# Optimization experiments

Measured on AMD Instinct MI355X. Metric: run time of the kernel, lower is better.

## Reference

```python
import jax, jax.numpy as jnp
import numpy as np

N_ING, N_DIR = 100000, 50000
E = 1000000
H, D = 4, 16          # heads, per-head dim
HID = H * D           # 64
LAT, COND = 32, 8
F_ING, F_DIR = 16, 8
OUT_ING = 16


def _han_edge(x_src, x_dst, att_s, att_d, edge_index, n_dst):
    # HANConv per-edge-type attention message passing.
    src, dst = edge_index[0], edge_index[1]
    a = jax.nn.leaky_relu(
        jnp.einsum('nhd,hd->nh', x_src, att_s)[src]
        + jnp.einsum('nhd,hd->nh', x_dst, att_d)[dst],
        negative_slope=0.2)                               # [E, H]
    amax = jax.ops.segment_max(a, dst, num_segments=n_dst)
    ex = jnp.exp(a - amax[dst])
    denom = jax.ops.segment_sum(ex, dst, num_segments=n_dst)
    alpha = ex / (denom[dst] + 1e-16)                     # PyG softmax eps
    out = jax.ops.segment_sum(x_src[src] * alpha[:, :, None], dst,
                              num_segments=n_dst)         # [n_dst, H, D]
    return jax.nn.relu(out.reshape(n_dst, HID))


def _group(outs, q, Wk, bk):
    # HANConv semantic-level attention across edge types.
    s = jnp.stack(outs)                                   # [T, N, HID]
    score = jnp.tanh(s @ Wk + bk).mean(axis=1) @ q        # [T]
    attn = jax.nn.softmax(score)
    return jnp.einsum('t,tnf->nf', attn, s)


def setup_inputs() -> dict:
    key = jax.random.key(0)
    ks = jax.random.split(key, 32)
    def ei(k, n_src, n_dst):
        k1, k2 = jax.random.split(k)
        return jnp.stack([jax.random.randint(k1, (E,), 0, n_src),
                          jax.random.randint(k2, (E,), 0, n_dst)]).astype(jnp.int64)
    s = 0.1
    inp = {
        'x_ing': jax.random.normal(ks[0], (N_ING, F_ING), jnp.float32),
        'x_dir': jax.random.normal(ks[1], (N_DIR, F_DIR), jnp.float32),
        'cond':  jax.random.normal(ks[2], (COND,), jnp.float32),
        'eps':   jax.random.normal(ks[3], (1, LAT), jnp.float32),
        'ei_cooc':     ei(ks[4], N_ING, N_DIR),
        'ei_used':     ei(ks[5], N_ING, N_DIR),
        'ei_contains': ei(ks[6], N_DIR, N_ING),
        'ei_pairs':    ei(ks[7], N_DIR, N_DIR),
        'ei_follows':  ei(ks[8], N_DIR, N_DIR),
        # node-type projections
        'W_pi': jax.random.normal(ks[9],  (F_ING, HID)) * s,
        'b_pi': jnp.zeros((HID,)),
        'W_pd': jax.random.normal(ks[10], (F_DIR, HID)) * s,
        'b_pd': jnp.zeros((HID,)),
        # semantic attention
        'Wk': jax.random.normal(ks[21], (HID, HID)) * s,
        'bk': jnp.zeros((HID,)),
        'q':  jax.random.normal(ks[22], (HID,)) * s,
        # VAE heads (input: 2*HID + COND)
        'W_mu': jax.random.normal(ks[23], (2 * HID + COND, LAT)) * s,
        'b_mu': jnp.zeros((LAT,)),
        'W_lv': jax.random.normal(ks[24], (2 * HID + COND, LAT)) * s,
        'b_lv': jnp.zeros((LAT,)),
        # decoder (fc1 is dead code in the original forward)
        'W_fc3': jax.random.normal(ks[25], (LAT, HID)) * s,
        'b_fc3': jnp.zeros((HID,)),
        'W_fc2': jax.random.normal(ks[26], (HID, OUT_ING)) * s,
        'b_fc2': jnp.zeros((OUT_ING,)),
    }
    for i, name in enumerate(['cooc', 'used', 'contains', 'pairs', 'follows']):
        inp[f'as_{name}'] = jax.random.normal(ks[11 + i], (H, D)) * s
        inp[f'ad_{name}'] = jax.random.normal(ks[16 + i], (H, D)) * s
    return inp


def reference(x_ing, x_dir, cond, eps,
              ei_cooc, ei_used, ei_contains, ei_pairs, ei_follows,
              W_pi, b_pi, W_pd, b_pd,
              as_cooc, ad_cooc, as_used, ad_used, as_contains, ad_contains,
              as_pairs, ad_pairs, as_follows, ad_follows,
              Wk, bk, q, W_mu, b_mu, W_lv, b_lv,
              W_fc3, b_fc3, W_fc2, b_fc2):
    # node-type projections -> [N, H, D]
    h_ing = (x_ing @ W_pi + b_pi).reshape(N_ING, H, D)
    h_dir = (x_dir @ W_pd + b_pd).reshape(N_DIR, H, D)

    o_cooc = _han_edge(h_ing, h_dir, as_cooc, ad_cooc, ei_cooc, N_DIR)
    o_used = _han_edge(h_ing, h_dir, as_used, ad_used, ei_used, N_DIR)
    o_cont = _han_edge(h_dir, h_ing, as_contains, ad_contains, ei_contains, N_ING)
    o_pair = _han_edge(h_dir, h_dir, as_pairs, ad_pairs, ei_pairs, N_DIR)
    o_foll = _han_edge(h_dir, h_dir, as_follows, ad_follows, ei_follows, N_DIR)

    out_ing = _group([o_cont], q, Wk, bk)                       # [N_ING, HID]
    out_dir = _group([o_cooc, o_used, o_pair, o_foll], q, Wk, bk)

    ingre_pool = out_ing.mean(axis=0, keepdims=True)            # [1, HID]
    direc_pool = out_dir.mean(axis=0, keepdims=True)
    graph_repr = jnp.concatenate([ingre_pool, direc_pool, cond[None]], axis=1)

    mu = graph_repr @ W_mu + b_mu
    logvar = graph_repr @ W_lv + b_lv
    z = mu + eps * jnp.exp(0.5 * logvar)

    # decoder: fc1 branch is overwritten in the original; effective path below
    recon = jnp.tanh(jax.nn.relu(z @ W_fc3 + b_fc3) @ W_fc2 + b_fc2)  # [1, OUT_ING]
    return recon, mu, logvar
```

## Files before the change

kernel.cpp:

```cpp
#include <hip/hip_runtime.h>
#include <hip/hip_fp16.h>
#include <math.h>

#define N_ING 100000
#define N_DIR 50000
#define NE    1000000
#define NDST_TOTAL 300000
#define NBUCK 1172
#define BA    64
#define NBK   (5 * BA)
#define I4PT  (NE / 4)
#define PB_ING 384
#define PB_DIR 192
#define LOG2E 1.442695041f

typedef float v2f __attribute__((ext_vector_type(2)));
typedef __attribute__((ext_vector_type(8))) short bf16x8;
typedef __attribute__((ext_vector_type(4))) float f32x4;

__global__ __launch_bounds__(256) void kA_kernel(
    const int* __restrict__ e0, const int* __restrict__ e1,
    const int* __restrict__ e2, const int* __restrict__ e3,
    const int* __restrict__ e4, int* __restrict__ blockcnt,
    const float* __restrict__ x_ing, const float* __restrict__ W_pi,
    const float* __restrict__ b_pi,
    const float* __restrict__ as_cooc, const float* __restrict__ as_used,
    const float* __restrict__ ad_contains,
    unsigned* __restrict__ h8_ing, __half* __restrict__ s_ing,
    const float* __restrict__ x_dir, const float* __restrict__ W_pd,
    const float* __restrict__ b_pd,
    const float* __restrict__ ad_cooc, const float* __restrict__ ad_used,
    const float* __restrict__ as_contains, const float* __restrict__ as_pairs,
    const float* __restrict__ ad_pairs, const float* __restrict__ as_follows,
    const float* __restrict__ ad_follows,
    unsigned* __restrict__ h8_dir, __half* __restrict__ s_dir)
{
    __shared__ int hist[NBUCK];
    __shared__ float sW[16 * 64];
    __shared__ float sbb[64];
    __shared__ float satt[7 * 64];
    __shared__ float sx[4][16];
    __shared__ float srow[4][64];

    const int bid = blockIdx.x;
    const int tid = threadIdx.x;
    if (bid < NBK) {
        const int type = bid / BA, blk = bid % BA;
        const int* ei = type == 0 ? e0 : type == 1 ? e1 : type == 2 ? e2
                      : type == 3 ? e3 : e4;
        const int base = type == 0 ? 0 : type == 1 ? 50000 : type == 2 ? 100000
                       : type == 3 ? 200000 : 250000;
        for (int i = tid; i < NBUCK; i += 256) hist[i] = 0;
        __syncthreads();
        const int4* d4 = (const int4*)(ei + NE);
        for (int i = blk * 256 + tid; i < I4PT; i += BA * 256) {
            int4 d = d4[i];
            atomicAdd(&hist[(base + d.x) >> 8], 1);
            atomicAdd(&hist[(base + d.y) >> 8], 1);
            atomicAdd(&hist[(base + d.z) >> 8], 1);
            atomicAdd(&hist[(base + d.w) >> 8], 1);
        }
        __syncthreads();
        int* row = blockcnt + (size_t)bid * NBUCK;
        for (int i = tid; i < NBUCK; i += 256) row[i] = hist[i];
    } else if (bid < NBK + PB_ING) {
        const int g = tid >> 6, t = tid & 63;
        for (int i = tid; i < 16 * 64; i += 256) sW[i] = W_pi[i];
        if (tid < 64) {
            sbb[tid] = b_pi[tid];
            satt[tid]       = as_cooc[tid] * LOG2E;
            satt[64 + tid]  = as_used[tid] * LOG2E;
            satt[128 + tid] = ad_contains[tid] * LOG2E;
        }
        __syncthreads();
        for (int q = bid - NBK; q < N_ING / 4; q += PB_ING) {
            int n = q * 4 + g;
            if (t < 16) sx[g][t] = x_ing[(size_t)n * 16 + t];
            __syncthreads();
            float s = sbb[t];
#pragma unroll
            for (int i = 0; i < 16; ++i) s += sx[g][i] * sW[i * 64 + t];
            srow[g][t] = s;
            __syncthreads();
            if (t < 16) {
                int w0 = __builtin_amdgcn_cvt_pk_fp8_f32(srow[g][t * 4], srow[g][t * 4 + 1], 0, false);
                int w  = __builtin_amdgcn_cvt_pk_fp8_f32(srow[g][t * 4 + 2], srow[g][t * 4 + 3], w0, true);
                h8_ing[(size_t)n * 16 + t] = (unsigned)w;
            }
            if (t < 12) {
                int slot = t >> 2, hh = t & 3;
                float sc = 0.f;
#pragma unroll
                for (int d = 0; d < 16; ++d)
                    sc += srow[g][hh * 16 + d] * satt[slot * 64 + hh * 16 + d];
                s_ing[(size_t)n * 12 + t] = __float2half(sc);
            }
            __syncthreads();
        }
    } else {
        const int g = tid >> 6, t = tid & 63;
        for (int i = tid; i < 8 * 64; i += 256) sW[i] = W_pd[i];
        if (tid < 64) {
            sbb[tid] = b_pd[tid];
            satt[tid]        = ad_cooc[tid] * LOG2E;
            satt[64  + tid]  = ad_used[tid] * LOG2E;
            satt[128 + tid]  = as_contains[tid] * LOG2E;
            satt[192 + tid]  = as_pairs[tid] * LOG2E;
            satt[256 + tid]  = ad_pairs[tid] * LOG2E;
            satt[320 + tid]  = as_follows[tid] * LOG2E;
            satt[384 + tid]  = ad_follows[tid] * LOG2E;
        }
        __syncthreads();
        for (int q = bid - NBK - PB_ING; q < N_DIR / 4; q += PB_DIR) {
            int n = q * 4 + g;
            if (t < 8) sx[g][t] = x_dir[(size_t)n * 8 + t];
            __syncthreads();
            float s = sbb[t];
#pragma unroll
            for (int i = 0; i < 8; ++i) s += sx[g][i] * sW[i * 64 + t];
            srow[g][t] = s;
            __syncthreads();
            if (t < 16) {
                int w0 = __builtin_amdgcn_cvt_pk_fp8_f32(srow[g][t * 4], srow[g][t * 4 + 1], 0, false);
                int w  = __builtin_amdgcn_cvt_pk_fp8_f32(srow[g][t * 4 + 2], srow[g][t * 4 + 3], w0, true);
                h8_dir[(size_t)n * 16 + t] = (unsigned)w;
            }
            if (t < 28) {
                int slot = t >> 2, hh = t & 3;
                float sc = 0.f;
#pragma unroll
                for (int d = 0; d < 16; ++d)
                    sc += srow[g][hh * 16 + d] * satt[slot * 64 + hh * 16 + d];
                s_dir[(size_t)n * 28 + t] = __float2half(sc);
            }
            __syncthreads();
        }
    }
}

__global__ __launch_bounds__(256) void k2_kernel(
    const int* __restrict__ blockcnt, int* __restrict__ blockbase,
    int* __restrict__ bbase, int* __restrict__ btot, int* __restrict__ cursor)
{
    __shared__ int part[4][64];
    __shared__ int tots[64];
    __shared__ int scn[64];
    __shared__ int bw;
    const int tid = threadIdx.x;
    const int kq = tid >> 6, bl = tid & 63;
    const int b = blockIdx.x * 64 + bl;
    const int K = NBK / 4;
    int ps = 0;
    if (b < NBUCK)
        for (int k = kq * K; k < kq * K + K; ++k)
            ps += blockcnt[(size_t)k * NBUCK + b];
    part[kq][bl] = ps;
    __syncthreads();
    if (tid < 64) {
        int t = part[0][tid] + part[1][tid] + part[2][tid] + part[3][tid];
        tots[tid] = t;
        scn[tid] = t;
    }
    __syncthreads();
    for (int off = 1; off < 64; off <<= 1) {
        int v = 0;
        if (tid < 64 && tid >= off) v = scn[tid - off];
        __syncthreads();
        if (tid < 64) scn[tid] += v;
        __syncthreads();
    }
    if (tid == 63) bw = atomicAdd(cursor, scn[63]);
    __syncthreads();
    if (b < NBUCK) {
        int bs = bw + scn[bl] - tots[bl];
        if (kq == 0) {
            bbase[b] = bs;
            btot[b] = tots[bl];
        }
        int run = bs;
        for (int q = 0; q < kq; ++q) run += part[q][bl];
        for (int k = kq * K; k < kq * K + K; ++k) {
            blockbase[(size_t)k * NBUCK + b] = run;
            run += blockcnt[(size_t)k * NBUCK + b];
        }
    }
}

__global__ __launch_bounds__(256) void k3_kernel(
    const int* __restrict__ e0, const int* __restrict__ e1,
    const int* __restrict__ e2, const int* __restrict__ e3,
    const int* __restrict__ e4, const int* __restrict__ blockbase,
    unsigned* __restrict__ bpair)
{
    __shared__ int cur[NBUCK];
    const int bid = blockIdx.x, tid = threadIdx.x;
    const int type = bid / BA, blk = bid % BA;
    const int* ei = type == 0 ? e0 : type == 1 ? e1 : type == 2 ? e2
                  : type == 3 ? e3 : e4;
    const int base = type == 0 ? 0 : type == 1 ? 50000 : type == 2 ? 100000
                   : type == 3 ? 200000 : 250000;
    const int* row = blockbase + (size_t)bid * NBUCK;
    for (int i = tid; i < NBUCK; i += 256) cur[i] = row[i];
    __syncthreads();
    const int4* s4 = (const int4*)ei;
    const int4* d4 = (const int4*)(ei + NE);
    for (int i = blk * 256 + tid; i < I4PT; i += BA * 256) {
        int4 s = s4[i];
        int4 d = d4[i];
        int g0 = base + d.x, g1 = base + d.y, g2 = base + d.z, g3 = base + d.w;
        int p0 = atomicAdd(&cur[g0 >> 8], 1);
        int p1 = atomicAdd(&cur[g1 >> 8], 1);
        int p2 = atomicAdd(&cur[g2 >> 8], 1);
        int p3 = atomicAdd(&cur[g3 >> 8], 1);
        bpair[p0] = ((unsigned)(g0 & 255) << 17) | (unsigned)s.x;
        bpair[p1] = ((unsigned)(g1 & 255) << 17) | (unsigned)s.y;
        bpair[p2] = ((unsigned)(g2 & 255) << 17) | (unsigned)s.z;
        bpair[p3] = ((unsigned)(g3 & 255) << 17) | (unsigned)s.w;
    }
}

__global__ __launch_bounds__(256) void k4_kernel(
    const unsigned* __restrict__ bpair, const int* __restrict__ bbase,
    const int* __restrict__ btot, int* __restrict__ perm,
    int* __restrict__ start, int* __restrict__ cnt)
{
    __shared__ int h[256], sc[256], cu[256];
    const int b = blockIdx.x, tid = threadIdx.x;
    const int jb = bbase[b], n = btot[b];
    h[tid] = 0;
    __syncthreads();
    for (int i = tid; i < n; i += 256)
        atomicAdd(&h[bpair[jb + i] >> 17], 1);
    __syncthreads();
    int v = h[tid];
    sc[tid] = v;
    __syncthreads();
    for (int off = 1; off < 256; off <<= 1) {
        int t2 = 0;
        if (tid >= off) t2 = sc[tid - off];
        __syncthreads();
        sc[tid] += t2;
        __syncthreads();
    }
    int ex = sc[tid] - v;
    cu[tid] = ex;
    int dg = b * 256 + tid;
    if (dg < NDST_TOTAL) {
        start[dg] = jb + ex;
        cnt[dg] = v;
    }
    __syncthreads();
    for (int i = tid; i < n; i += 256) {
        unsigned p = bpair[jb + i];
        int pos = atomicAdd(&cu[p >> 17], 1);
        perm[jb + pos] = (int)(p & 0x1FFFF);
    }
}

__global__ __launch_bounds__(256) void agg_all_kernel(
    const int* __restrict__ perm, const int* __restrict__ start,
    const int* __restrict__ cnttot,
    const unsigned* __restrict__ h8_ing, const unsigned* __restrict__ h8_dir,
    const __half* __restrict__ s_ing, const __half* __restrict__ s_dir,
    unsigned* __restrict__ rows8,
    float* __restrict__ pool_ing, float* __restrict__ pool_dir)
{
    __shared__ __align__(16) float srow[4][64];
    __shared__ float sred[4][64];
    const int t = threadIdx.x & 63, w = threadIdx.x >> 6;
    const int g  = t >> 4;
    const int l4 = t & 15;
    const int hq = l4 >> 2;

    float p_ing = 0.f;
    float p0 = 0.f, p1 = 0.f, p2 = 0.f, p3 = 0.f;
    const int nwaves = gridDim.x * 4;
    for (int d = blockIdx.x * 4 + w; d < NDST_TOTAL; d += nwaves) {
        int type, ld;
        const __half *ssrc, *sdst;
        const unsigned* hsrc;
        unsigned uss, uds; int soff, doff;
        if (d < 50000)       { type = 0; ld = d;          ssrc = s_ing; uss = 12; soff = 0;  sdst = s_dir; uds = 28; doff = 0;  hsrc = h8_ing; }
        else if (d < 100000) { type = 1; ld = d - 50000;  ssrc = s_ing; uss = 12; soff = 4;  sdst = s_dir; uds = 28; doff = 4;  hsrc = h8_ing; }
        else if (d < 200000) { type = 2; ld = d - 100000; ssrc = s_dir; uss = 28; soff = 8;  sdst = s_ing; uds = 12; doff = 8;  hsrc = h8_dir; }
        else if (d < 250000) { type = 3; ld = d - 200000; ssrc = s_dir; uss = 28; soff = 12; sdst = s_dir; uds = 28; doff = 16; hsrc = h8_dir; }
        else                 { type = 4; ld = d - 250000; ssrc = s_dir; uss = 28; soff = 20; sdst = s_dir; uds = 28; doff = 24; hsrc = h8_dir; }
        float adst = __half2float(sdst[(unsigned)ld * uds + (unsigned)(doff + hq)]);
        const unsigned usoff = (unsigned)(soff + hq);
        int jb = start[d], je = jb + cnttot[d];
        int jl = je - 1;
        float4 acc = make_float4(0.f, 0.f, 0.f, 0.f);
        float dsum = 0.f;
        for (int j = jb; j < je; j += 16) {
            int j0 = j + g, j1 = j + 4 + g, j2 = j + 8 + g, j3 = j + 12 + g;
            bool v0 = j0 < je, v1 = j1 < je, v2 = j2 < je, v3 = j3 < je;
            unsigned s0 = (unsigned)perm[v0 ? j0 : jl];
            unsigned s1 = (unsigned)perm[v1 ? j1 : jl];
            unsigned s2 = (unsigned)perm[v2 ? j2 : jl];
            unsigned s3 = (unsigned)perm[v3 ? j3 : jl];
            float c0 = __half2float(ssrc[s0 * uss + usoff]);
            float c1 = __half2float(ssrc[s1 * uss + usoff]);
            float c2 = __half2float(ssrc[s2 * uss + usoff]);
            float c3 = __half2float(ssrc[s3 * uss + usoff]);
            unsigned u0 = hsrc[s0 * 16u + (unsigned)l4];
            unsigned u1 = hsrc[s1 * 16u + (unsigned)l4];
            unsigned u2 = hsrc[s2 * 16u + (unsigned)l4];
            unsigned u3 = hsrc[s3 * 16u + (unsigned)l4];
            float a0 = c0 + adst; a0 = a0 > 0.f ? a0 : 0.2f * a0;
            float a1 = c1 + adst; a1 = a1 > 0.f ? a1 : 0.2f * a1;
            float a2 = c2 + adst; a2 = a2 > 0.f ? a2 : 0.2f * a2;
            float a3 = c3 + adst; a3 = a3 > 0.f ? a3 : 0.2f * a3;
            float e0 = v0 ? __builtin_amdgcn_exp2f(a0) : 0.f;
            float e1 = v1 ? __builtin_amdgcn_exp2f(a1) : 0.f;
            float e2 = v2 ? __builtin_amdgcn_exp2f(a2) : 0.f;
            float e3 = v3 ? __builtin_amdgcn_exp2f(a3) : 0.f;
            dsum += (e0 + e1) + (e2 + e3);
            v2f lo0 = __builtin_amdgcn_cvt_pk_f32_fp8((int)u0, false);
            v2f hi0 = __builtin_amdgcn_cvt_pk_f32_fp8((int)u0, true);
            v2f lo1 = __builtin_amdgcn_cvt_pk_f32_fp8((int)u1, false);
            v2f hi1 = __builtin_amdgcn_cvt_pk_f32_fp8((int)u1, true);
            v2f lo2 = __builtin_amdgcn_cvt_pk_f32_fp8((int)u2, false);
            v2f hi2 = __builtin_amdgcn_cvt_pk_f32_fp8((int)u2, true);
            v2f lo3 = __builtin_amdgcn_cvt_pk_f32_fp8((int)u3, false);
            v2f hi3 = __builtin_amdgcn_cvt_pk_f32_fp8((int)u3, true);
            acc.x += (lo0.x * e0 + lo1.x * e1) + (lo2.x * e2 + lo3.x * e3);
            acc.y += (lo0.y * e0 + lo1.y * e1) + (lo2.y * e2 + lo3.y * e3);
            acc.z += (hi0.x * e0 + hi1.x * e1) + (hi2.x * e2 + hi3.x * e3);
            acc.w += (hi0.y * e0 + hi1.y * e1) + (hi2.y * e2 + hi3.y * e3);
        }
#pragma unroll
        for (int mask = 16; mask <= 32; mask <<= 1) {
            acc.x += __shfl_xor(acc.x, mask, 64);
            acc.y += __shfl_xor(acc.y, mask, 64);
            acc.z += __shfl_xor(acc.z, mask, 64);
            acc.w += __shfl_xor(acc.w, mask, 64);
            dsum  += __shfl_xor(dsum,  mask, 64);
        }
        float inv = 1.f / (dsum + 1e-16f);
        float4 v4 = make_float4(fmaxf(acc.x * inv, 0.f), fmaxf(acc.y * inv, 0.f),
                                fmaxf(acc.z * inv, 0.f), fmaxf(acc.w * inv, 0.f));
        if (g == 0) *(float4*)&srow[w][l4 * 4] = v4;
        float v = srow[w][t];
        if (type == 2) {
            p_ing += v;
        } else {
            if (type == 0)      p0 += v;
            else if (type == 1) p1 += v;
            else if (type == 3) p2 += v;
            else                p3 += v;
            if (g == 0) {
                unsigned md = (unsigned)(d < 100000 ? d : d - 100000);
                int r0 = __builtin_amdgcn_cvt_pk_fp8_f32(v4.x, v4.y, 0, false);
                int r1 = __builtin_amdgcn_cvt_pk_fp8_f32(v4.z, v4.w, r0, true);
                rows8[md * 16u + (unsigned)l4] = (unsigned)r1;
            }
        }
    }
    float vals[5] = { p_ing, p0, p1, p2, p3 };
    float* outs[5] = { pool_ing, pool_dir, pool_dir + 64, pool_dir + 128,
                       pool_dir + 192 };
    for (int i = 0; i < 5; ++i) {
        __syncthreads();
        sred[w][t] = vals[i];
        __syncthreads();
        if (w == 0)
            atomicAdd(&outs[i][t], sred[0][t] + sred[1][t] + sred[2][t] + sred[3][t]);
    }
}

__global__ __launch_bounds__(256) void sem_kernel(
    const unsigned* __restrict__ rows8, const float* __restrict__ Wk,
    const float* __restrict__ bk, float* __restrict__ sem_dir)
{
    __shared__ float swk[4096];
    __shared__ float ssem[256];
    const int tid = threadIdx.x;
    for (int i = tid; i < 4096; i += 256) swk[i] = Wk[i];
    ssem[tid] = 0.f;
    __syncthreads();

    const int lane = tid & 63, w = tid >> 6;
    const int col = lane & 15, kg = lane >> 4;

    bf16x8 bfr[4][2];
    float biasv[4];
#pragma unroll
    for (int nt = 0; nt < 4; ++nt) {
        biasv[nt] = bk[nt * 16 + col];
#pragma unroll
        for (int ks = 0; ks < 2; ++ks) {
            bf16x8 bb;
#pragma unroll
            for (int j = 0; j < 8; ++j) {
                int k = ks * 32 + kg * 8 + j;
                unsigned u = __builtin_bit_cast(unsigned, swk[k * 64 + nt * 16 + col]);
                u = u + 0x7FFFu + ((u >> 16) & 1u);
                bb[j] = (short)(u >> 16);
            }
            bfr[nt][ks] = bb;
        }
    }

    const int gw = blockIdx.x * 4 + w;
    const int nw = gridDim.x * 4;
    for (int tile = gw; tile < 12500; tile += nw) {
        const int tt = tile / 3125;
        const unsigned* rp = rows8 + (unsigned)(tile * 16 + col) * 16u;
        bf16x8 afr[2];
#pragma unroll
        for (int ks = 0; ks < 2; ++ks) {
            uint2 uu = *(const uint2*)(rp + ks * 8 + kg * 2);
            v2f l0 = __builtin_amdgcn_cvt_pk_f32_fp8((int)uu.x, false);
            v2f h0 = __builtin_amdgcn_cvt_pk_f32_fp8((int)uu.x, true);
            v2f l1 = __builtin_amdgcn_cvt_pk_f32_fp8((int)uu.y, false);
            v2f h1 = __builtin_amdgcn_cvt_pk_f32_fp8((int)uu.y, true);
            bf16x8 aa;
            aa[0] = (short)(__builtin_bit_cast(unsigned, l0.x) >> 16);
            aa[1] = (short)(__builtin_bit_cast(unsigned, l0.y) >> 16);
            aa[2] = (short)(__builtin_bit_cast(unsigned, h0.x) >> 16);
            aa[3] = (short)(__builtin_bit_cast(unsigned, h0.y) >> 16);
            aa[4] = (short)(__builtin_bit_cast(unsigned, l1.x) >> 16);
            aa[5] = (short)(__builtin_bit_cast(unsigned, l1.y) >> 16);
            aa[6] = (short)(__builtin_bit_cast(unsigned, h1.x) >> 16);
            aa[7] = (short)(__builtin_bit_cast(unsigned, h1.y) >> 16);
            afr[ks] = aa;
        }
#pragma unroll
        for (int nt = 0; nt < 4; ++nt) {
            f32x4 acc = {0.f, 0.f, 0.f, 0.f};
            acc = __builtin_amdgcn_mfma_f32_16x16x32_bf16(afr[0], bfr[nt][0], acc, 0, 0, 0);
            acc = __builtin_amdgcn_mfma_f32_16x16x32_bf16(afr[1], bfr[nt][1], acc, 0, 0, 0);
            float s = 0.f;
#pragma unroll
            for (int reg = 0; reg < 4; ++reg) {
                float x = acc[reg] + biasv[nt];
                x = fminf(fmaxf(x, -15.f), 15.f);
                float e = __builtin_amdgcn_exp2f(x * (2.f * LOG2E));
                s += (e - 1.f) * __builtin_amdgcn_rcpf(e + 1.f);
            }
            s += __shfl_xor(s, 16, 64);
            s += __shfl_xor(s, 32, 64);
            if (lane < 16) atomicAdd(&ssem[tt * 64 + nt * 16 + col], s);
        }
    }
    __syncthreads();
    atomicAdd(&sem_dir[tid], ssem[tid]);
}

__global__ __launch_bounds__(64) void final_kernel(
    const float* __restrict__ pool_ing, const float* __restrict__ pool_dir,
    const float* __restrict__ sem_dir, const float* __restrict__ q,
    const float* __restrict__ cond, const float* __restrict__ eps,
    const float* __restrict__ W_mu, const float* __restrict__ b_mu,
    const float* __restrict__ W_lv, const float* __restrict__ b_lv,
    const float* __restrict__ W_fc3, const float* __restrict__ b_fc3,
    const float* __restrict__ W_fc2, const float* __restrict__ b_fc2,
    float* __restrict__ out)
{
    __shared__ float gr[136];
    __shared__ float sc[4], attn[4];
    __shared__ float z[32], hfc[64];
    int t = threadIdx.x;
    if (t < 4) {
        float s = 0.f;
        for (int f = 0; f < 64; ++f)
            s += (sem_dir[t * 64 + f] / (float)N_DIR) * q[f];
        sc[t] = s;
    }
    gr[t] = pool_ing[t] / (float)N_ING;
    __syncthreads();
    if (t == 0) {
        float m = fmaxf(fmaxf(sc[0], sc[1]), fmaxf(sc[2], sc[3]));
        float ssum = 0.f;
        for (int i = 0; i < 4; ++i) { attn[i] = expf(sc[i] - m); ssum += attn[i]; }
        for (int i = 0; i < 4; ++i) attn[i] /= ssum;
    }
    __syncthreads();
    {
        float v = 0.f;
        for (int tt = 0; tt < 4; ++tt)
            v += attn[tt] * (pool_dir[tt * 64 + t] / (float)N_DIR);
        gr[64 + t] = v;
    }
    if (t < 8) gr[128 + t] = cond[t];
    __syncthreads();
    if (t < 32) {
        float m = b_mu[t], lv = b_lv[t];
        for (int i = 0; i < 136; ++i) {
            float g = gr[i];
            m  += g * W_mu[i * 32 + t];
            lv += g * W_lv[i * 32 + t];
        }
        out[16 + t] = m;
        out[48 + t] = lv;
        z[t] = m + eps[t] * expf(0.5f * lv);
    }
    __syncthreads();
    {
        float v = b_fc3[t];
        for (int j = 0; j < 32; ++j) v += z[j] * W_fc3[j * 64 + t];
        hfc[t] = fmaxf(v, 0.f);
    }
    __syncthreads();
    if (t < 16) {
        float v = b_fc2[t];
        for (int f = 0; f < 64; ++f) v += hfc[f] * W_fc2[f * 16 + t];
        out[t] = tanhf(v);
    }
}

extern "C" void kernel_launch(void* const* d_in, const int* in_sizes, int n_in,
                              void* d_out, int out_size, void* d_ws, size_t ws_size,
                              hipStream_t stream) {
    const float* x_ing = (const float*)d_in[0];
    const float* x_dir = (const float*)d_in[1];
    const float* cond  = (const float*)d_in[2];
    const float* eps   = (const float*)d_in[3];
    const int* ei_cooc     = (const int*)d_in[4];
    const int* ei_used     = (const int*)d_in[5];
    const int* ei_contains = (const int*)d_in[6];
    const int* ei_pairs    = (const int*)d_in[7];
    const int* ei_follows  = (const int*)d_in[8];
    const float* W_pi = (const float*)d_in[9];
    const float* b_pi = (const float*)d_in[10];
    const float* W_pd = (const float*)d_in[11];
    const float* b_pd = (const float*)d_in[12];
    const float* Wk   = (const float*)d_in[13];
    const float* bk   = (const float*)d_in[14];
    const float* q    = (const float*)d_in[15];
    const float* W_mu = (const float*)d_in[16];
    const float* b_mu = (const float*)d_in[17];
    const float* W_lv = (const float*)d_in[18];
    const float* b_lv = (const float*)d_in[19];
    const float* W_fc3 = (const float*)d_in[20];
    const float* b_fc3 = (const float*)d_in[21];
    const float* W_fc2 = (const float*)d_in[22];
    const float* b_fc2 = (const float*)d_in[23];
    const float* as_cooc     = (const float*)d_in[24];
    const float* ad_cooc     = (const float*)d_in[25];
    const float* as_used     = (const float*)d_in[26];
    const float* ad_used     = (const float*)d_in[27];
    const float* as_contains = (const float*)d_in[28];
    const float* ad_contains = (const float*)d_in[29];
    const float* as_pairs    = (const float*)d_in[30];
    const float* ad_pairs    = (const float*)d_in[31];
    const float* as_follows  = (const float*)d_in[32];
    const float* ad_follows  = (const float*)d_in[33];

    unsigned* bpair = (unsigned*)d_ws;
    unsigned* h8_ing = bpair + (size_t)5 * NE;
    unsigned* h8_dir = h8_ing + (size_t)N_ING * 16;
    __half* s_ing = (__half*)(h8_dir + (size_t)N_DIR * 16);
    __half* s_dir = s_ing + (size_t)N_ING * 12;
    int*   perm  = (int*)(s_dir + (size_t)N_DIR * 28);
    int*   bbase  = perm + (size_t)5 * NE;
    int*   btot   = bbase + NBUCK;
    int*   start  = btot + NBUCK;
    int*   cnt    = start + NDST_TOTAL;
    int*   cursor = cnt + NDST_TOTAL;
    float* pool_ing = (float*)(cursor + 1);
    float* pool_dir = pool_ing + 64;
    float* sem_dir  = pool_dir + 256;
    unsigned* rows8 = bpair;
    int* blockcnt  = (int*)bpair;
    int* blockbase = (int*)perm;

    hipMemsetAsync(cursor, 0, (1 + 64 + 256 + 256) * sizeof(int), stream);

    kA_kernel<<<NBK + PB_ING + PB_DIR, 256, 0, stream>>>(
        ei_cooc, ei_used, ei_contains, ei_pairs, ei_follows, blockcnt,
        x_ing, W_pi, b_pi, as_cooc, as_used, ad_contains, h8_ing, s_ing,
        x_dir, W_pd, b_pd, ad_cooc, ad_used, as_contains, as_pairs, ad_pairs,
        as_follows, ad_follows, h8_dir, s_dir);

    k2_kernel<<<(NBUCK + 63) / 64, 256, 0, stream>>>(
        blockcnt, blockbase, bbase, btot, cursor);

    k3_kernel<<<NBK, 256, 0, stream>>>(
        ei_cooc, ei_used, ei_contains, ei_pairs, ei_follows, blockbase, bpair);

    k4_kernel<<<NBUCK, 256, 0, stream>>>(bpair, bbase, btot, perm, start, cnt);

    agg_all_kernel<<<2048, 256, 0, stream>>>(
        perm, start, cnt, h8_ing, h8_dir, s_ing, s_dir, rows8,
        pool_ing, pool_dir);

    sem_kernel<<<512, 256, 0, stream>>>(rows8, Wk, bk, sem_dir);

    final_kernel<<<1, 64, 0, stream>>>(
        pool_ing, pool_dir, sem_dir, q, cond, eps,
        W_mu, b_mu, W_lv, b_lv, W_fc3, b_fc3, W_fc2, b_fc2, (float*)d_out);
}
```

Before: 494.4 us.

## Widen sort buckets to 512 destinations and restructure aggregation gather per edge

Doubles the bucket width of the two-level counting sort from 256 to 512 destinations, which halves the bucket count and so the per-block histogram and scan sizes. Each bucket is also padded to a multiple of 16 entries, which keeps bucket starts aligned. The aggregation kernel changes its lane mapping: a team of four lanes handles one edge and loads 16 bytes of the fp8 row per lane, instead of 16 lanes each loading 4 bytes across four edges. This trades more registers and longer shuffle reductions for fewer, wider gather loads and a vectorised row write.

```diff
diff --git a/kernel.cpp b/kernel.cpp
--- a/kernel.cpp
+++ b/kernel.cpp
@@ -6,12 +6,15 @@
 #define N_DIR 50000
 #define NE    1000000
 #define NDST_TOTAL 300000
-#define NBUCK 1172
+#define NBUCK 586
+#define BSH   9
+#define BMSK  511
 #define BA    64
 #define NBK   (5 * BA)
 #define I4PT  (NE / 4)
 #define PB_ING 384
 #define PB_DIR 192
+#define BPAIR_CAP (5 * NE + 16 * NBUCK)
 #define LOG2E 1.442695041f
 
 typedef float v2f __attribute__((ext_vector_type(2)));
@@ -55,10 +58,10 @@
         const int4* d4 = (const int4*)(ei + NE);
         for (int i = blk * 256 + tid; i < I4PT; i += BA * 256) {
             int4 d = d4[i];
-            atomicAdd(&hist[(base + d.x) >> 8], 1);
-            atomicAdd(&hist[(base + d.y) >> 8], 1);
-            atomicAdd(&hist[(base + d.z) >> 8], 1);
-            atomicAdd(&hist[(base + d.w) >> 8], 1);
+            atomicAdd(&hist[(base + d.x) >> BSH], 1);
+            atomicAdd(&hist[(base + d.y) >> BSH], 1);
+            atomicAdd(&hist[(base + d.z) >> BSH], 1);
+            atomicAdd(&hist[(base + d.w) >> BSH], 1);
         }
         __syncthreads();
         int* row = blockcnt + (size_t)bid * NBUCK;
@@ -159,7 +162,7 @@
     if (tid < 64) {
         int t = part[0][tid] + part[1][tid] + part[2][tid] + part[3][tid];
         tots[tid] = t;
-        scn[tid] = t;
+        scn[tid] = (t + 15) & ~15;
     }
     __syncthreads();
     for (int off = 1; off < 64; off <<= 1) {
@@ -172,7 +175,8 @@
     if (tid == 63) bw = atomicAdd(cursor, scn[63]);
     __syncthreads();
     if (b < NBUCK) {
-        int bs = bw + scn[bl] - tots[bl];
+        int pad = (tots[bl] + 15) & ~15;
+        int bs = bw + scn[bl] - pad;
         if (kq == 0) {
             bbase[b] = bs;
             btot[b] = tots[bl];
@@ -208,14 +212,14 @@
         int4 s = s4[i];
         int4 d = d4[i];
         int g0 = base + d.x, g1 = base + d.y, g2 = base + d.z, g3 = base + d.w;
-        int p0 = atomicAdd(&cur[g0 >> 8], 1);
-        int p1 = atomicAdd(&cur[g1 >> 8], 1);
-        int p2 = atomicAdd(&cur[g2 >> 8], 1);
-        int p3 = atomicAdd(&cur[g3 >> 8], 1);
-        bpair[p0] = ((unsigned)(g0 & 255) << 17) | (unsigned)s.x;
-        bpair[p1] = ((unsigned)(g1 & 255) << 17) | (unsigned)s.y;
-        bpair[p2] = ((unsigned)(g2 & 255) << 17) | (unsigned)s.z;
-        bpair[p3] = ((unsigned)(g3 & 255) << 17) | (unsigned)s.w;
+        int p0 = atomicAdd(&cur[g0 >> BSH], 1);
+        int p1 = atomicAdd(&cur[g1 >> BSH], 1);
+        int p2 = atomicAdd(&cur[g2 >> BSH], 1);
+        int p3 = atomicAdd(&cur[g3 >> BSH], 1);
+        bpair[p0] = ((unsigned)(g0 & BMSK) << 17) | (unsigned)s.x;
+        bpair[p1] = ((unsigned)(g1 & BMSK) << 17) | (unsigned)s.y;
+        bpair[p2] = ((unsigned)(g2 & BMSK) << 17) | (unsigned)s.z;
+        bpair[p3] = ((unsigned)(g3 & BMSK) << 17) | (unsigned)s.w;
     }
 }
 
@@ -224,31 +228,32 @@
     const int* __restrict__ btot, int* __restrict__ perm,
     int* __restrict__ start, int* __restrict__ cnt)
 {
-    __shared__ int h[256], sc[256], cu[256];
+    __shared__ int h[512], cu[512];
+    __shared__ int ts[256];
     const int b = blockIdx.x, tid = threadIdx.x;
     const int jb = bbase[b], n = btot[b];
     h[tid] = 0;
+    h[tid + 256] = 0;
     __syncthreads();
     for (int i = tid; i < n; i += 256)
         atomicAdd(&h[bpair[jb + i] >> 17], 1);
     __syncthreads();
-    int v = h[tid];
-    sc[tid] = v;
+    int v0 = h[2 * tid], v1 = h[2 * tid + 1];
+    ts[tid] = v0 + v1;
     __syncthreads();
     for (int off = 1; off < 256; off <<= 1) {
         int t2 = 0;
-        if (tid >= off) t2 = sc[tid - off];
-        __syncthreads();
-        sc[tid] += t2;
-        __syncthreads();
-    }
-    int ex = sc[tid] - v;
-    cu[tid] = ex;
-    int dg = b * 256 + tid;
-    if (dg < NDST_TOTAL) {
-        start[dg] = jb + ex;
-        cnt[dg] = v;
-    }
+        if (tid >= off) t2 = ts[tid - off];
+        __syncthreads();
+        ts[tid] += t2;
+        __syncthreads();
+    }
+    int ex = ts[tid] - (v0 + v1);
+    cu[2 * tid] = ex;
+    cu[2 * tid + 1] = ex + v0;
+    int dg = b * 512 + 2 * tid;
+    if (dg < NDST_TOTAL) { start[dg] = jb + ex; cnt[dg] = v0; }
+    if (dg + 1 < NDST_TOTAL) { start[dg + 1] = jb + ex + v0; cnt[dg + 1] = v1; }
     __syncthreads();
     for (int i = tid; i < n; i += 256) {
         unsigned p = bpair[jb + i];
@@ -268,9 +273,8 @@
     __shared__ __align__(16) float srow[4][64];
     __shared__ float sred[4][64];
     const int t = threadIdx.x & 63, w = threadIdx.x >> 6;
-    const int g  = t >> 4;
-    const int l4 = t & 15;
-    const int hq = l4 >> 2;
+    const int team = t >> 2;
+    const int f    = t & 3;
 
     float p_ing = 0.f;
     float p0 = 0.f, p1 = 0.f, p2 = 0.f, p3 = 0.f;
@@ -285,61 +289,65 @@
         else if (d < 200000) { type = 2; ld = d - 100000; ssrc = s_dir; uss = 28; soff = 8;  sdst = s_ing; uds = 12; doff = 8;  hsrc = h8_dir; }
         else if (d < 250000) { type = 3; ld = d - 200000; ssrc = s_dir; uss = 28; soff = 12; sdst = s_dir; uds = 28; doff = 16; hsrc = h8_dir; }
         else                 { type = 4; ld = d - 250000; ssrc = s_dir; uss = 28; soff = 20; sdst = s_dir; uds = 28; doff = 24; hsrc = h8_dir; }
-        float adst = __half2float(sdst[(unsigned)ld * uds + (unsigned)(doff + hq)]);
-        const unsigned usoff = (unsigned)(soff + hq);
+        float adst = __half2float(sdst[(unsigned)ld * uds + (unsigned)(doff + f)]);
+        const unsigned usoff = (unsigned)(soff + f);
         int jb = start[d], je = jb + cnttot[d];
         int jl = je - 1;
-        float4 acc = make_float4(0.f, 0.f, 0.f, 0.f);
+        float4 aa = make_float4(0.f, 0.f, 0.f, 0.f);
+        float4 bb = make_float4(0.f, 0.f, 0.f, 0.f);
+        float4 cc = make_float4(0.f, 0.f, 0.f, 0.f);
+        float4 dd = make_float4(0.f, 0.f, 0.f, 0.f);
         float dsum = 0.f;
         for (int j = jb; j < je; j += 16) {
-            int j0 = j + g, j1 = j + 4 + g, j2 = j + 8 + g, j3 = j + 12 + g;
-            bool v0 = j0 < je, v1 = j1 < je, v2 = j2 < je, v3 = j3 < je;
-            unsigned s0 = (unsigned)perm[v0 ? j0 : jl];
-            unsigned s1 = (unsigned)perm[v1 ? j1 : jl];
-            unsigned s2 = (unsigned)perm[v2 ? j2 : jl];
-            unsigned s3 = (unsigned)perm[v3 ? j3 : jl];
+            int jj = j + team;
+            bool valid = jj < je;
+            unsigned s0 = (unsigned)perm[valid ? jj : jl];
             float c0 = __half2float(ssrc[s0 * uss + usoff]);
-            float c1 = __half2float(ssrc[s1 * uss + usoff]);
-            float c2 = __half2float(ssrc[s2 * uss + usoff]);
-            float c3 = __half2float(ssrc[s3 * uss + usoff]);
-            unsigned u0 = hsrc[s0 * 16u + (unsigned)l4];
-            unsigned u1 = hsrc[s1 * 16u + (unsigned)l4];
-            unsigned u2 = hsrc[s2 * 16u + (unsigned)l4];
-            unsigned u3 = hsrc[s3 * 16u + (unsigned)l4];
-            float a0 = c0 + adst; a0 = a0 > 0.f ? a0 : 0.2f * a0;
-            float a1 = c1 + adst; a1 = a1 > 0.f ? a1 : 0.2f * a1;
-            float a2 = c2 + adst; a2 = a2 > 0.f ? a2 : 0.2f * a2;
-            float a3 = c3 + adst; a3 = a3 > 0.f ? a3 : 0.2f * a3;
-            float e0 = v0 ? __builtin_amdgcn_exp2f(a0) : 0.f;
-            float e1 = v1 ? __builtin_amdgcn_exp2f(a1) : 0.f;
-            float e2 = v2 ? __builtin_amdgcn_exp2f(a2) : 0.f;
-            float e3 = v3 ? __builtin_amdgcn_exp2f(a3) : 0.f;
-            dsum += (e0 + e1) + (e2 + e3);
-            v2f lo0 = __builtin_amdgcn_cvt_pk_f32_fp8((int)u0, false);
-            v2f hi0 = __builtin_amdgcn_cvt_pk_f32_fp8((int)u0, true);
-            v2f lo1 = __builtin_amdgcn_cvt_pk_f32_fp8((int)u1, false);
-            v2f hi1 = __builtin_amdgcn_cvt_pk_f32_fp8((int)u1, true);
-            v2f lo2 = __builtin_amdgcn_cvt_pk_f32_fp8((int)u2, false);
-            v2f hi2 = __builtin_amdgcn_cvt_pk_f32_fp8((int)u2, true);
-            v2f lo3 = __builtin_amdgcn_cvt_pk_f32_fp8((int)u3, false);
-            v2f hi3 = __builtin_amdgcn_cvt_pk_f32_fp8((int)u3, true);
-            acc.x += (lo0.x * e0 + lo1.x * e1) + (lo2.x * e2 + lo3.x * e3);
-            acc.y += (lo0.y * e0 + lo1.y * e1) + (lo2.y * e2 + lo3.y * e3);
-            acc.z += (hi0.x * e0 + hi1.x * e1) + (hi2.x * e2 + hi3.x * e3);
-            acc.w += (hi0.y * e0 + hi1.y * e1) + (hi2.y * e2 + hi3.y * e3);
-        }
-#pragma unroll
-        for (int mask = 16; mask <= 32; mask <<= 1) {
-            acc.x += __shfl_xor(acc.x, mask, 64);
-            acc.y += __shfl_xor(acc.y, mask, 64);
-            acc.z += __shfl_xor(acc.z, mask, 64);
-            acc.w += __shfl_xor(acc.w, mask, 64);
-            dsum  += __shfl_xor(dsum,  mask, 64);
+            uint4 u = *(const uint4*)(hsrc + s0 * 16u + (unsigned)(f * 4));
+            float a0 = c0 + adst;
+            a0 = fmaxf(a0, 0.2f * a0);
+            float e0 = valid ? __builtin_amdgcn_exp2f(a0) : 0.f;
+            dsum += e0;
+            v2f lx = __builtin_amdgcn_cvt_pk_f32_fp8((int)u.x, false);
+            v2f hx = __builtin_amdgcn_cvt_pk_f32_fp8((int)u.x, true);
+            v2f ly = __builtin_amdgcn_cvt_pk_f32_fp8((int)u.y, false);
+            v2f hy = __builtin_amdgcn_cvt_pk_f32_fp8((int)u.y, true);
+            v2f lz = __builtin_amdgcn_cvt_pk_f32_fp8((int)u.z, false);
+            v2f hz = __builtin_amdgcn_cvt_pk_f32_fp8((int)u.z, true);
+            v2f lw = __builtin_amdgcn_cvt_pk_f32_fp8((int)u.w, false);
+            v2f hw = __builtin_amdgcn_cvt_pk_f32_fp8((int)u.w, true);
+            aa.x += lx.x * e0; aa.y += lx.y * e0; aa.z += hx.x * e0; aa.w += hx.y * e0;
+            bb.x += ly.x * e0; bb.y += ly.y * e0; bb.z += hy.x * e0; bb.w += hy.y * e0;
+            cc.x += lz.x * e0; cc.y += lz.y * e0; cc.z += hz.x * e0; cc.w += hz.y * e0;
+            dd.x += lw.x * e0; dd.y += lw.y * e0; dd.z += hw.x * e0; dd.w += hw.y * e0;
+        }
+#pragma unroll
+        for (int mask = 4; mask <= 32; mask <<= 1) {
+            aa.x += __shfl_xor(aa.x, mask, 64); aa.y += __shfl_xor(aa.y, mask, 64);
+            aa.z += __shfl_xor(aa.z, mask, 64); aa.w += __shfl_xor(aa.w, mask, 64);
+            bb.x += __shfl_xor(bb.x, mask, 64); bb.y += __shfl_xor(bb.y, mask, 64);
+            bb.z += __shfl_xor(bb.z, mask, 64); bb.w += __shfl_xor(bb.w, mask, 64);
+            cc.x += __shfl_xor(cc.x, mask, 64); cc.y += __shfl_xor(cc.y, mask, 64);
+            cc.z += __shfl_xor(cc.z, mask, 64); cc.w += __shfl_xor(cc.w, mask, 64);
+            dd.x += __shfl_xor(dd.x, mask, 64); dd.y += __shfl_xor(dd.y, mask, 64);
+            dd.z += __shfl_xor(dd.z, mask, 64); dd.w += __shfl_xor(dd.w, mask, 64);
+            dsum += __shfl_xor(dsum, mask, 64);
         }
         float inv = 1.f / (dsum + 1e-16f);
-        float4 v4 = make_float4(fmaxf(acc.x * inv, 0.f), fmaxf(acc.y * inv, 0.f),
-                                fmaxf(acc.z * inv, 0.f), fmaxf(acc.w * inv, 0.f));
-        if (g == 0) *(float4*)&srow[w][l4 * 4] = v4;
+        aa.x = fmaxf(aa.x * inv, 0.f); aa.y = fmaxf(aa.y * inv, 0.f);
+        aa.z = fmaxf(aa.z * inv, 0.f); aa.w = fmaxf(aa.w * inv, 0.f);
+        bb.x = fmaxf(bb.x * inv, 0.f); bb.y = fmaxf(bb.y * inv, 0.f);
+        bb.z = fmaxf(bb.z * inv, 0.f); bb.w = fmaxf(bb.w * inv, 0.f);
+        cc.x = fmaxf(cc.x * inv, 0.f); cc.y = fmaxf(cc.y * inv, 0.f);
+        cc.z = fmaxf(cc.z * inv, 0.f); cc.w = fmaxf(cc.w * inv, 0.f);
+        dd.x = fmaxf(dd.x * inv, 0.f); dd.y = fmaxf(dd.y * inv, 0.f);
+        dd.z = fmaxf(dd.z * inv, 0.f); dd.w = fmaxf(dd.w * inv, 0.f);
+        if (t < 4) {
+            *(float4*)&srow[w][t * 16]      = aa;
+            *(float4*)&srow[w][t * 16 + 4]  = bb;
+            *(float4*)&srow[w][t * 16 + 8]  = cc;
+            *(float4*)&srow[w][t * 16 + 12] = dd;
+        }
         float v = srow[w][t];
         if (type == 2) {
             p_ing += v;
@@ -348,11 +356,18 @@
             else if (type == 1) p1 += v;
             else if (type == 3) p2 += v;
             else                p3 += v;
-            if (g == 0) {
+            if (t < 4) {
                 unsigned md = (unsigned)(d < 100000 ? d : d - 100000);
-                int r0 = __builtin_amdgcn_cvt_pk_fp8_f32(v4.x, v4.y, 0, false);
-                int r1 = __builtin_amdgcn_cvt_pk_fp8_f32(v4.z, v4.w, r0, true);
-                rows8[md * 16u + (unsigned)l4] = (unsigned)r1;
+                uint4 r;
+                int x0 = __builtin_amdgcn_cvt_pk_fp8_f32(aa.x, aa.y, 0, false);
+                r.x = (unsigned)__builtin_amdgcn_cvt_pk_fp8_f32(aa.z, aa.w, x0, true);
+                int y0 = __builtin_amdgcn_cvt_pk_fp8_f32(bb.x, bb.y, 0, false);
+                r.y = (unsigned)__builtin_amdgcn_cvt_pk_fp8_f32(bb.z, bb.w, y0, true);
+                int z0 = __builtin_amdgcn_cvt_pk_fp8_f32(cc.x, cc.y, 0, false);
+                r.z = (unsigned)__builtin_amdgcn_cvt_pk_fp8_f32(cc.z, cc.w, z0, true);
+                int w0 = __builtin_amdgcn_cvt_pk_fp8_f32(dd.x, dd.y, 0, false);
+                r.w = (unsigned)__builtin_amdgcn_cvt_pk_fp8_f32(dd.z, dd.w, w0, true);
+                *(uint4*)(rows8 + md * 16u + (unsigned)(t * 4)) = r;
             }
         }
     }
@@ -548,12 +563,12 @@
     const float* ad_follows  = (const float*)d_in[33];
 
     unsigned* bpair = (unsigned*)d_ws;
-    unsigned* h8_ing = bpair + (size_t)5 * NE;
+    unsigned* h8_ing = bpair + (size_t)BPAIR_CAP;
     unsigned* h8_dir = h8_ing + (size_t)N_ING * 16;
     __half* s_ing = (__half*)(h8_dir + (size_t)N_DIR * 16);
     __half* s_dir = s_ing + (size_t)N_ING * 12;
     int*   perm  = (int*)(s_dir + (size_t)N_DIR * 28);
-    int*   bbase  = perm + (size_t)5 * NE;
+    int*   bbase  = perm + (size_t)BPAIR_CAP;
     int*   btot   = bbase + NBUCK;
     int*   start  = btot + NBUCK;
     int*   cnt    = start + NDST_TOTAL;
```

New measurement: 588.3 us. 19.0% more time.

## Use 512-destination buckets with 16-aligned bucket bases in the CSR build

Applied to the files above, without the earlier changes.

Doubles the destination-bucket width from 256 to 512 and halves the bucket count, so the per-block histogram and blockcnt/blockbase tables shrink and the scan does less work. Each bucket's base offset is padded to a multiple of 16 elements to give aligned segments, and the workspace arrays grow to absorb the padding. The per-bucket sort kernel now handles two destinations per thread with a 512-entry local histogram, so each block does more serial work and LDS atomic contention per bucket may rise.

```diff
diff --git a/kernel.cpp b/kernel.cpp
--- a/kernel.cpp
+++ b/kernel.cpp
@@ -6,12 +6,15 @@
 #define N_DIR 50000
 #define NE    1000000
 #define NDST_TOTAL 300000
-#define NBUCK 1172
+#define NBUCK 586
+#define BSH   9
+#define BMSK  511
 #define BA    64
 #define NBK   (5 * BA)
 #define I4PT  (NE / 4)
 #define PB_ING 384
 #define PB_DIR 192
+#define BPAIR_CAP (5 * NE + 16 * NBUCK)
 #define LOG2E 1.442695041f
 
 typedef float v2f __attribute__((ext_vector_type(2)));
@@ -55,10 +58,10 @@
         const int4* d4 = (const int4*)(ei + NE);
         for (int i = blk * 256 + tid; i < I4PT; i += BA * 256) {
             int4 d = d4[i];
-            atomicAdd(&hist[(base + d.x) >> 8], 1);
-            atomicAdd(&hist[(base + d.y) >> 8], 1);
-            atomicAdd(&hist[(base + d.z) >> 8], 1);
-            atomicAdd(&hist[(base + d.w) >> 8], 1);
+            atomicAdd(&hist[(base + d.x) >> BSH], 1);
+            atomicAdd(&hist[(base + d.y) >> BSH], 1);
+            atomicAdd(&hist[(base + d.z) >> BSH], 1);
+            atomicAdd(&hist[(base + d.w) >> BSH], 1);
         }
         __syncthreads();
         int* row = blockcnt + (size_t)bid * NBUCK;
@@ -159,7 +162,7 @@
     if (tid < 64) {
         int t = part[0][tid] + part[1][tid] + part[2][tid] + part[3][tid];
         tots[tid] = t;
-        scn[tid] = t;
+        scn[tid] = (t + 15) & ~15;
     }
     __syncthreads();
     for (int off = 1; off < 64; off <<= 1) {
@@ -172,7 +175,8 @@
     if (tid == 63) bw = atomicAdd(cursor, scn[63]);
     __syncthreads();
     if (b < NBUCK) {
-        int bs = bw + scn[bl] - tots[bl];
+        int pad = (tots[bl] + 15) & ~15;
+        int bs = bw + scn[bl] - pad;
         if (kq == 0) {
             bbase[b] = bs;
             btot[b] = tots[bl];
@@ -208,14 +212,14 @@
         int4 s = s4[i];
         int4 d = d4[i];
         int g0 = base + d.x, g1 = base + d.y, g2 = base + d.z, g3 = base + d.w;
-        int p0 = atomicAdd(&cur[g0 >> 8], 1);
-        int p1 = atomicAdd(&cur[g1 >> 8], 1);
-        int p2 = atomicAdd(&cur[g2 >> 8], 1);
-        int p3 = atomicAdd(&cur[g3 >> 8], 1);
-        bpair[p0] = ((unsigned)(g0 & 255) << 17) | (unsigned)s.x;
-        bpair[p1] = ((unsigned)(g1 & 255) << 17) | (unsigned)s.y;
-        bpair[p2] = ((unsigned)(g2 & 255) << 17) | (unsigned)s.z;
-        bpair[p3] = ((unsigned)(g3 & 255) << 17) | (unsigned)s.w;
+        int p0 = atomicAdd(&cur[g0 >> BSH], 1);
+        int p1 = atomicAdd(&cur[g1 >> BSH], 1);
+        int p2 = atomicAdd(&cur[g2 >> BSH], 1);
+        int p3 = atomicAdd(&cur[g3 >> BSH], 1);
+        bpair[p0] = ((unsigned)(g0 & BMSK) << 17) | (unsigned)s.x;
+        bpair[p1] = ((unsigned)(g1 & BMSK) << 17) | (unsigned)s.y;
+        bpair[p2] = ((unsigned)(g2 & BMSK) << 17) | (unsigned)s.z;
+        bpair[p3] = ((unsigned)(g3 & BMSK) << 17) | (unsigned)s.w;
     }
 }
 
@@ -224,31 +228,32 @@
     const int* __restrict__ btot, int* __restrict__ perm,
     int* __restrict__ start, int* __restrict__ cnt)
 {
-    __shared__ int h[256], sc[256], cu[256];
+    __shared__ int h[512], cu[512];
+    __shared__ int ts[256];
     const int b = blockIdx.x, tid = threadIdx.x;
     const int jb = bbase[b], n = btot[b];
     h[tid] = 0;
+    h[tid + 256] = 0;
     __syncthreads();
     for (int i = tid; i < n; i += 256)
         atomicAdd(&h[bpair[jb + i] >> 17], 1);
     __syncthreads();
-    int v = h[tid];
-    sc[tid] = v;
+    int v0 = h[2 * tid], v1 = h[2 * tid + 1];
+    ts[tid] = v0 + v1;
     __syncthreads();
     for (int off = 1; off < 256; off <<= 1) {
         int t2 = 0;
-        if (tid >= off) t2 = sc[tid - off];
-        __syncthreads();
-        sc[tid] += t2;
-        __syncthreads();
-    }
-    int ex = sc[tid] - v;
-    cu[tid] = ex;
-    int dg = b * 256 + tid;
-    if (dg < NDST_TOTAL) {
-        start[dg] = jb + ex;
-        cnt[dg] = v;
-    }
+        if (tid >= off) t2 = ts[tid - off];
+        __syncthreads();
+        ts[tid] += t2;
+        __syncthreads();
+    }
+    int ex = ts[tid] - (v0 + v1);
+    cu[2 * tid] = ex;
+    cu[2 * tid + 1] = ex + v0;
+    int dg = b * 512 + 2 * tid;
+    if (dg < NDST_TOTAL) { start[dg] = jb + ex; cnt[dg] = v0; }
+    if (dg + 1 < NDST_TOTAL) { start[dg + 1] = jb + ex + v0; cnt[dg + 1] = v1; }
     __syncthreads();
     for (int i = tid; i < n; i += 256) {
         unsigned p = bpair[jb + i];
@@ -548,12 +553,12 @@
     const float* ad_follows  = (const float*)d_in[33];
 
     unsigned* bpair = (unsigned*)d_ws;
-    unsigned* h8_ing = bpair + (size_t)5 * NE;
+    unsigned* h8_ing = bpair + (size_t)BPAIR_CAP;
     unsigned* h8_dir = h8_ing + (size_t)N_ING * 16;
     __half* s_ing = (__half*)(h8_dir + (size_t)N_DIR * 16);
     __half* s_dir = s_ing + (size_t)N_ING * 12;
     int*   perm  = (int*)(s_dir + (size_t)N_DIR * 28);
-    int*   bbase  = perm + (size_t)5 * NE;
+    int*   bbase  = perm + (size_t)BPAIR_CAP;
     int*   btot   = bbase + NBUCK;
     int*   start  = btot + NBUCK;
     int*   cnt    = start + NDST_TOTAL;
```

After: 491.6 us. About the same (-0.6%).
